# Kernel tuning notes

Hardware: AMD Instinct MI355X
Metric: run time of the kernel (lower is better)

## Reference

```python
import jax, jax.numpy as jnp
import numpy as np
import math

D_MODEL = 1024
NUM_HEADS = 16
D_K = D_MODEL // NUM_HEADS
B, S = 2, 2048


def setup_inputs() -> dict:
    key = jax.random.key(0)
    ks = jax.random.split(key, 11)
    scale = 1.0 / math.sqrt(D_MODEL)
    inp = {
        "query": jax.random.normal(ks[0], (B, S, D_MODEL), jnp.float32),
        "key": jax.random.normal(ks[1], (B, S, D_MODEL), jnp.float32),
        "value": jax.random.normal(ks[2], (B, S, D_MODEL), jnp.float32),
        "Wq": jax.random.normal(ks[3], (D_MODEL, D_MODEL), jnp.float32) * scale,
        "bq": jnp.zeros((D_MODEL,), jnp.float32),
        "Wk": jax.random.normal(ks[4], (D_MODEL, D_MODEL), jnp.float32) * scale,
        "bk": jnp.zeros((D_MODEL,), jnp.float32),
        "Wv": jax.random.normal(ks[5], (D_MODEL, D_MODEL), jnp.float32) * scale,
        "bv": jnp.zeros((D_MODEL,), jnp.float32),
        "Wo": jax.random.normal(ks[6], (D_MODEL, D_MODEL), jnp.float32) * scale,
        "bo": jnp.zeros((D_MODEL,), jnp.float32),
    }
    return inp


def reference(query, key, value, Wq, bq, Wk, bk, Wv, bv, Wo, bo):
    b, s, _ = query.shape
    # QKV projections (torch Linear: x @ W.T + b)
    Q = query @ Wq.T + bq
    K = key @ Wk.T + bk
    V = value @ Wv.T + bv
    # [b, h, s, d_k]
    Q = Q.reshape(b, s, NUM_HEADS, D_K).transpose(0, 2, 1, 3)
    K = K.reshape(b, s, NUM_HEADS, D_K).transpose(0, 2, 1, 3)
    V = V.reshape(b, s, NUM_HEADS, D_K).transpose(0, 2, 1, 3)
    score = jnp.einsum("bhqd,bhkd->bhqk", Q, K) / math.sqrt(D_K)
    attn = jax.nn.softmax(score, axis=-1)
    out = jnp.einsum("bhqk,bhkd->bhqd", attn, V)
    out = out.transpose(0, 2, 1, 3).reshape(b, s, D_MODEL)
    return out @ Wo.T + bo
```

## Files before the change

### kernel.cpp

```cpp
#include <hip/hip_runtime.h>

#define NHEADS 16
#define SEQ    2048
#define BATCH  2
#define DMODEL 1024
#define MTOT   4096

typedef __attribute__((ext_vector_type(8)))  short short8;
typedef __attribute__((ext_vector_type(4)))  float f32x4;
typedef __attribute__((ext_vector_type(16))) float f32x16;

__device__ __forceinline__ unsigned short f32_to_bf16_rn(float x) {
  unsigned int u = __float_as_uint(x);
  u += 0x7fffu + ((u >> 16) & 1u);
  return (unsigned short)(u >> 16);
}

__device__ __forceinline__ unsigned cvt_pk_bf16(float lo, float hi_) {
  unsigned r;
  asm("v_cvt_pk_bf16_f32 %0, %1, %2" : "=v"(r) : "v"(lo), "v"(hi_));
  return r;
}

__device__ __forceinline__ void permlane32_swap(unsigned &a, unsigned &b) {
  asm("v_permlane32_swap_b32 %0, %1" : "+v"(a), "+v"(b));
}

__device__ __forceinline__ void async16(void* lds, const void* g) {
  __builtin_amdgcn_global_load_lds((const __attribute__((address_space(1))) unsigned int*)g,
                                   (__attribute__((address_space(3))) unsigned int*)lds, 16, 0, 0);
}

__global__ void cvt_bf16_kernel(const float* __restrict__ x0, const float* __restrict__ x1,
                                const float* __restrict__ x2,
                                const float* __restrict__ w0, const float* __restrict__ w1,
                                const float* __restrict__ w2, const float* __restrict__ w3,
                                unsigned short* __restrict__ obase)
{
  const int e = (blockIdx.x*256 + threadIdx.x)*8;
  const float* src;
  int local;
  if (e < 3*4194304) {
    const int t = e >> 22;
    src = t==0 ? x0 : t==1 ? x1 : x2;
    local = e & (4194304-1);
    src += local;
    local += t << 22;
  } else {
    const int f = e - 3*4194304;
    const int t = f >> 20;
    src = t==0 ? w0 : t==1 ? w1 : t==2 ? w2 : w3;
    src += (f & (1048576-1));
    local = e;
  }
  const float4 v0 = *(const float4*)(src);
  const float4 v1 = *(const float4*)(src + 4);
  union { unsigned short u[8]; uint4 v; } r;
  r.u[0] = f32_to_bf16_rn(v0.x); r.u[1] = f32_to_bf16_rn(v0.y);
  r.u[2] = f32_to_bf16_rn(v0.z); r.u[3] = f32_to_bf16_rn(v0.w);
  r.u[4] = f32_to_bf16_rn(v1.x); r.u[5] = f32_to_bf16_rn(v1.y);
  r.u[6] = f32_to_bf16_rn(v1.z); r.u[7] = f32_to_bf16_rn(v1.w);
  *(uint4*)(obase + local) = r.v;
}

template<int BM>
__device__ __forceinline__ void gemm_core(const unsigned short* __restrict__ A,
                                          const unsigned short* __restrict__ W,
                                          unsigned short* sA, unsigned short* sB,
                                          int m0, int n0, f32x4 (&acc)[BM/32][4])
{
  constexpr int MI = BM/32;
  const int t = threadIdx.x;
  const int lane = t & 63;
  const int wv = t >> 6;
  const int wm = wv >> 1, wn = wv & 1;
  const int lr = lane & 15, lk = lane >> 4;

  for (int kt = 0; kt < DMODEL/64; ++kt) {
    #pragma unroll
    for (int g = 0; g < MI; ++g) {
      const int o  = g*4096 + t*16;
      const int so = o ^ (((o >> 7) & 7) << 4);
      const int row = so >> 7, colE = (so & 127) >> 1;
      async16((char*)sA + o, A + (size_t)(m0 + row)*DMODEL + kt*64 + colE);
    }
    #pragma unroll
    for (int g = 0; g < 4; ++g) {
      const int o  = g*4096 + t*16;
      const int so = o ^ (((o >> 7) & 7) << 4);
      const int row = so >> 7, colE = (so & 127) >> 1;
      async16((char*)sB + o, W + (size_t)(n0 + row)*DMODEL + kt*64 + colE);
    }
    __syncthreads();
    #pragma unroll
    for (int ks = 0; ks < 2; ++ks) {
      short8 af[MI], bf[4];
      #pragma unroll
      for (int mi = 0; mi < MI; ++mi) {
        const int row = wm*(BM/2) + mi*16 + lr;
        const int sl  = (ks*4 + lk) ^ (row & 7);
        af[mi] = *(const short8*)(sA + row*64 + sl*8);
      }
      #pragma unroll
      for (int ni = 0; ni < 4; ++ni) {
        const int row = wn*64 + ni*16 + lr;
        const int sl  = (ks*4 + lk) ^ (row & 7);
        bf[ni] = *(const short8*)(sB + row*64 + sl*8);
      }
      #pragma unroll
      for (int mi = 0; mi < MI; ++mi)
        #pragma unroll
        for (int ni = 0; ni < 4; ++ni)
          acc[mi][ni] = __builtin_amdgcn_mfma_f32_16x16x32_bf16(af[mi], bf[ni], acc[mi][ni], 0, 0, 0);
    }
    __syncthreads();
  }
}

__global__ __launch_bounds__(256, 2)
void qkv_gemm_kernel(const unsigned short* __restrict__ Xq, const unsigned short* __restrict__ Xk,
                     const unsigned short* __restrict__ Xv,
                     const unsigned short* __restrict__ Wq, const unsigned short* __restrict__ Wk,
                     const unsigned short* __restrict__ Wv,
                     const float* __restrict__ bq, const float* __restrict__ bk,
                     const float* __restrict__ bv,
                     unsigned short* __restrict__ Qp, unsigned short* __restrict__ Kp,
                     unsigned short* __restrict__ Vtp)
{
  constexpr int BM = 128;
  constexpr int MI = BM/32;
  __shared__ __align__(16) unsigned short smem[17024];
  unsigned short* sA = smem;
  unsigned short* sB = smem + 8192;

  const int m0   = blockIdx.x * BM;
  const int nabs = blockIdx.y * 128;
  const int wsel = nabs >> 10;
  const int n0   = nabs & 1023;
  const unsigned short* A = wsel==0 ? Xq : wsel==1 ? Xk : Xv;
  const unsigned short* W = wsel==0 ? Wq : wsel==1 ? Wk : Wv;
  const float* bias       = wsel==0 ? bq : wsel==1 ? bk : bv;

  f32x4 acc[MI][4];
  #pragma unroll
  for (int mi = 0; mi < MI; ++mi)
    #pragma unroll
    for (int ni = 0; ni < 4; ++ni)
      acc[mi][ni] = {0.f, 0.f, 0.f, 0.f};

  gemm_core<BM>(A, W, sA, sB, m0, n0, acc);

  const int t = threadIdx.x, lane = t & 63, wvx = t >> 6;
  const int wm = wvx >> 1, wn = wvx & 1;
  const int lr = lane & 15, lk = lane >> 4;

  if (wsel == 2) {
    #pragma unroll
    for (int ni = 0; ni < 4; ++ni) {
      const float badd = bias[n0 + wn*64 + ni*16 + lr];
      #pragma unroll
      for (int mi = 0; mi < MI; ++mi)
        #pragma unroll
        for (int r = 0; r < 4; ++r) {
          const int ml = wm*(BM/2) + mi*16 + lk*4 + r;
          smem[(wn*64 + ni*16 + lr)*132 + ml] = f32_to_bf16_rn(acc[mi][ni][r] + badd);
        }
    }
    __syncthreads();
    const int bb = m0 >> 11, s0 = m0 & 2047;
    const int jr = (t & 15)*8, nr = t >> 4;
    #pragma unroll
    for (int pass = 0; pass < 8; ++pass) {
      const int n  = pass*16 + nr;
      const int nn = n0 + n, hh = nn >> 6, d = nn & 63;
      const short8 v = *(const short8*)(smem + n*132 + jr);
      *(short8*)(Vtp + (((size_t)bb*NHEADS + hh)*64 + d)*SEQ + s0 + jr) = v;
    }
  } else {
    unsigned short* dst = wsel==0 ? Qp : Kp;
    const float qscale = (wsel == 0) ? 0.125f * 1.4426950408889634f : 1.0f;
    #pragma unroll
    for (int ni = 0; ni < 4; ++ni) {
      const int nn = n0 + wn*64 + ni*16 + lr;
      const float badd = bias[nn];
      const int hh = nn >> 6, d = nn & 63;
      #pragma unroll
      for (int mi = 0; mi < MI; ++mi) {
        #pragma unroll
        for (int r = 0; r < 4; ++r) {
          const int m = m0 + wm*(BM/2) + mi*16 + lk*4 + r;
          const int bb = m >> 11, s = m & 2047;
          const float v = (acc[mi][ni][r] + badd) * qscale;
          dst[(((size_t)bb*NHEADS + hh)*SEQ + s)*64 + d] = f32_to_bf16_rn(v);
        }
      }
    }
  }
}

__global__ __launch_bounds__(256, 2)
void attn_kernel(const unsigned short* __restrict__ Qp, const unsigned short* __restrict__ Kp,
                 const unsigned short* __restrict__ Vtp, unsigned short* __restrict__ Op)
{
  __shared__ __align__(16) unsigned short sm[3*8192];
  constexpr int NT = SEQ/64;

  const int t = threadIdx.x, lane = t & 63, w = t >> 6;
  const int lq = lane & 31, hi = lane >> 5;
  const int f   = blockIdx.x + 16*blockIdx.y + 256*blockIdx.z;
  const int wid = (f & 7)*64 + (f >> 3);
  const int qt = wid & 15, h = (wid >> 4) & 15, b = wid >> 8;

  const size_t bh = (size_t)b*NHEADS + h;
  const unsigned short* Qh = Qp  + bh*SEQ*64;
  const unsigned short* Kh = Kp  + bh*SEQ*64;
  const unsigned short* Vh = Vtp + bh*64*SEQ;
  const int q0 = qt*128 + w*32;

  short8 qf[4];
  #pragma unroll
  for (int ks = 0; ks < 4; ++ks)
    qf[ks] = *(const short8*)(Qh + (size_t)(q0 + lq)*64 + ks*16 + hi*8);

  union { unsigned u[4]; short8 s; } ones;
  #pragma unroll
  for (int i = 0; i < 4; ++i) ones.u[i] = 0x3F803F80u;

  const unsigned short* srcp;
  size_t sstride;
  if (w < 2) { srcp = Kh + (size_t)(w*32 + lq)*64 + hi*8;        sstride = 64*64; }
  else       { srcp = Vh + (size_t)((w-2)*32 + lq)*2048 + hi*8;  sstride = 64;    }

  #pragma unroll
  for (int i = 0; i < 4; ++i) async16((char*)sm + 0     + w*4096 + i*1024, srcp + i*16);
  srcp += sstride;
  #pragma unroll
  for (int i = 0; i < 4; ++i) async16((char*)sm + 16384 + w*4096 + i*1024, srcp + i*16);
  srcp += sstride;

  f32x16 o[2], ls, stA[2], stB[2];
  #pragma unroll
  for (int d = 0; d < 2; ++d)
    #pragma unroll
    for (int r = 0; r < 16; ++r) { o[d][r] = 0.f; stA[d][r] = 0.f; stB[d][r] = 0.f; }
  #pragma unroll
  for (int r = 0; r < 16; ++r) ls[r] = 0.f;

  asm volatile("s_waitcnt vmcnt(4)" ::: "memory");
  __syncthreads();
  __builtin_amdgcn_s_setprio(1);
  #pragma unroll
  for (int sub = 0; sub < 2; ++sub)
    #pragma unroll
    for (int ks = 0; ks < 4; ++ks) {
      const short8 kf = *(const short8*)(sm + (sub*4 + ks)*512 + lane*8);
      stA[sub] = __builtin_amdgcn_mfma_f32_32x32x16_bf16(kf, qf[ks], stA[sub], 0, 0, 0);
    }
  __builtin_amdgcn_s_setprio(0);

  auto body = [&](f32x16 (&cur)[2], f32x16 (&nxt)[2], int tc, int obC, int obN, int obS) {
    asm volatile("s_waitcnt vmcnt(0)" ::: "memory");
    __syncthreads();
    if (tc + 2 < NT) {
      #pragma unroll
      for (int i = 0; i < 4; ++i)
        async16((char*)sm + obS + w*4096 + i*1024, srcp + i*16);
      srcp += sstride;
    }
    if (tc + 1 < NT) {
      const unsigned short* kb = sm + (obN >> 1);
      #pragma unroll
      for (int s = 0; s < 2; ++s)
        #pragma unroll
        for (int r = 0; r < 16; ++r) nxt[s][r] = 0.f;
      __builtin_amdgcn_s_setprio(1);
      #pragma unroll
      for (int sub = 0; sub < 2; ++sub)
        #pragma unroll
        for (int ks = 0; ks < 4; ++ks) {
          const short8 kf = *(const short8*)(kb + (sub*4 + ks)*512 + lane*8);
          nxt[sub] = __builtin_amdgcn_mfma_f32_32x32x16_bf16(kf, qf[ks], nxt[sub], 0, 0, 0);
        }
      __builtin_amdgcn_s_setprio(0);
    }
    #pragma unroll
    for (int s = 0; s < 2; ++s)
      #pragma unroll
      for (int r = 0; r < 16; ++r)
        cur[s][r] = __builtin_amdgcn_exp2f(cur[s][r]);
    const unsigned short* vb = sm + (obC >> 1) + 4096;
    #pragma unroll
    for (int sub = 0; sub < 2; ++sub) {
      union { unsigned u[4]; short8 s; } pA, pB;
      {
        unsigned x0 = cvt_pk_bf16(cur[sub][0],  cur[sub][1]);
        unsigned x1 = cvt_pk_bf16(cur[sub][2],  cur[sub][3]);
        unsigned y0 = cvt_pk_bf16(cur[sub][4],  cur[sub][5]);
        unsigned y1 = cvt_pk_bf16(cur[sub][6],  cur[sub][7]);
        permlane32_swap(x0, y0);
        permlane32_swap(x1, y1);
        pA.u[0] = x0; pA.u[1] = x1; pA.u[2] = y0; pA.u[3] = y1;
        unsigned z0 = cvt_pk_bf16(cur[sub][8],  cur[sub][9]);
        unsigned z1 = cvt_pk_bf16(cur[sub][10], cur[sub][11]);
        unsigned w0 = cvt_pk_bf16(cur[sub][12], cur[sub][13]);
        unsigned w1 = cvt_pk_bf16(cur[sub][14], cur[sub][15]);
        permlane32_swap(z0, w0);
        permlane32_swap(z1, w1);
        pB.u[0] = z0; pB.u[1] = z1; pB.u[2] = w0; pB.u[3] = w1;
      }
      const short8 v00 = *(const short8*)(vb + (0*4 + 2*sub    )*512 + lane*8);
      const short8 v01 = *(const short8*)(vb + (0*4 + 2*sub + 1)*512 + lane*8);
      const short8 v10 = *(const short8*)(vb + (1*4 + 2*sub    )*512 + lane*8);
      const short8 v11 = *(const short8*)(vb + (1*4 + 2*sub + 1)*512 + lane*8);
      __builtin_amdgcn_s_setprio(1);
      o[0] = __builtin_amdgcn_mfma_f32_32x32x16_bf16(v00, pA.s, o[0], 0, 0, 0);
      o[1] = __builtin_amdgcn_mfma_f32_32x32x16_bf16(v10, pA.s, o[1], 0, 0, 0);
      ls   = __builtin_amdgcn_mfma_f32_32x32x16_bf16(ones.s, pA.s, ls, 0, 0, 0);
      o[0] = __builtin_amdgcn_mfma_f32_32x32x16_bf16(v01, pB.s, o[0], 0, 0, 0);
      o[1] = __builtin_amdgcn_mfma_f32_32x32x16_bf16(v11, pB.s, o[1], 0, 0, 0);
      ls   = __builtin_amdgcn_mfma_f32_32x32x16_bf16(ones.s, pB.s, ls, 0, 0, 0);
      __builtin_amdgcn_s_setprio(0);
    }
  };

  int obC = 0, obN = 16384, obS = 32768;
  for (int t2 = 0; t2 < NT; t2 += 2) {
    body(stA, stB, t2,     obC, obN, obS);
    int tmp = obC; obC = obN; obN = obS; obS = tmp;
    body(stB, stA, t2 + 1, obC, obN, obS);
    tmp = obC; obC = obN; obN = obS; obS = tmp;
  }

  const float inv = __builtin_amdgcn_rcpf(ls[0]);
  unsigned short* orow = Op + ((size_t)b*SEQ + q0 + lq)*DMODEL + h*64;
  #pragma unroll
  for (int dblk = 0; dblk < 2; ++dblk)
    #pragma unroll
    for (int g = 0; g < 4; ++g) {
      union { unsigned short us[4]; uint2 v; } pk;
      #pragma unroll
      for (int r = 0; r < 4; ++r) pk.us[r] = f32_to_bf16_rn(o[dblk][g*4 + r] * inv);
      *(uint2*)(orow + dblk*32 + g*8 + hi*4) = pk.v;
    }
}

__global__ __launch_bounds__(256, 2)
void oproj_gemm_kernel(const unsigned short* __restrict__ Oin, const unsigned short* __restrict__ Wo,
                       const float* __restrict__ bo, float* __restrict__ out)
{
  constexpr int BM = 64;
  constexpr int MI = BM/32;
  __shared__ __align__(16) unsigned short sA[BM*64];
  __shared__ __align__(16) unsigned short sB[128*64];
  const int m0 = blockIdx.x * BM;
  const int n0 = blockIdx.y * 128;

  f32x4 acc[MI][4];
  #pragma unroll
  for (int mi = 0; mi < MI; ++mi)
    #pragma unroll
    for (int ni = 0; ni < 4; ++ni)
      acc[mi][ni] = {0.f,0.f,0.f,0.f};

  gemm_core<BM>(Oin, Wo, sA, sB, m0, n0, acc);

  const int t = threadIdx.x, lane = t & 63, wvx = t >> 6;
  const int wm = wvx >> 1, wn = wvx & 1;
  const int lr = lane & 15, lk = lane >> 4;

  #pragma unroll
  for (int ni = 0; ni < 4; ++ni) {
    const int nn = n0 + wn*64 + ni*16 + lr;
    const float badd = bo[nn];
    #pragma unroll
    for (int mi = 0; mi < MI; ++mi)
      #pragma unroll
      for (int r = 0; r < 4; ++r) {
        const int m = m0 + wm*(BM/2) + mi*16 + lk*4 + r;
        out[(size_t)m*DMODEL + nn] = acc[mi][ni][r] + badd;
      }
  }
}

extern "C" void kernel_launch(void* const* d_in, const int* in_sizes, int n_in,
                              void* d_out, int out_size, void* d_ws, size_t ws_size,
                              hipStream_t stream) {
  const float* query = (const float*)d_in[0];
  const float* key   = (const float*)d_in[1];
  const float* value = (const float*)d_in[2];
  const float* Wq    = (const float*)d_in[3];
  const float* bq    = (const float*)d_in[4];
  const float* Wk    = (const float*)d_in[5];
  const float* bk    = (const float*)d_in[6];
  const float* Wv    = (const float*)d_in[7];
  const float* bv    = (const float*)d_in[8];
  const float* Wo    = (const float*)d_in[9];
  const float* bo    = (const float*)d_in[10];

  const size_t NX = (size_t)MTOT*DMODEL;
  const size_t NW = (size_t)DMODEL*DMODEL;
  unsigned short* w   = (unsigned short*)d_ws;
  unsigned short* Xq  = w;
  unsigned short* Xk  = Xq  + NX;
  unsigned short* Xv  = Xk  + NX;
  unsigned short* Wqp = Xv  + NX;
  unsigned short* Wkp = Wqp + NW;
  unsigned short* Wvp = Wkp + NW;
  unsigned short* Wop = Wvp + NW;
  unsigned short* Qp  = Wop + NW;
  unsigned short* Kp  = Qp  + NX;
  unsigned short* Vtp = Kp  + NX;
  unsigned short* Opb = Vtp + NX;

  cvt_bf16_kernel<<<dim3(8192), 256, 0, stream>>>(
      query, key, value, Wq, Wk, Wv, Wo, w);
  qkv_gemm_kernel<<<dim3(32, 24), 256, 0, stream>>>(
      Xq, Xk, Xv, Wqp, Wkp, Wvp, bq, bk, bv, Qp, Kp, Vtp);
  attn_kernel<<<dim3(16, 16, 2), 256, 0, stream>>>(Qp, Kp, Vtp, Opb);
  oproj_gemm_kernel<<<dim3(64, 8), 256, 0, stream>>>(Opb, Wop, bo, (float*)d_out);
}
```

Baseline: 113.0 us.

## Load K and V fragments directly from global into registers, dropping LDS staging

```diff
diff --git a/kernel.cpp b/kernel.cpp
--- a/kernel.cpp
+++ b/kernel.cpp
@@ -202,7 +202,6 @@
 void attn_kernel(const unsigned short* __restrict__ Qp, const unsigned short* __restrict__ Kp,
                  const unsigned short* __restrict__ Vtp, unsigned short* __restrict__ Op)
 {
-  __shared__ __align__(16) unsigned short sm[3*8192];
   constexpr int NT = SEQ/64;
 
   const int t = threadIdx.x, lane = t & 63, w = t >> 6;
@@ -226,109 +225,90 @@
   #pragma unroll
   for (int i = 0; i < 4; ++i) ones.u[i] = 0x3F803F80u;
 
-  const unsigned short* srcp;
-  size_t sstride;
-  if (w < 2) { srcp = Kh + (size_t)(w*32 + lq)*64 + hi*8;        sstride = 64*64; }
-  else       { srcp = Vh + (size_t)((w-2)*32 + lq)*2048 + hi*8;  sstride = 64;    }
-
-  #pragma unroll
-  for (int i = 0; i < 4; ++i) async16((char*)sm + 0     + w*4096 + i*1024, srcp + i*16);
-  srcp += sstride;
-  #pragma unroll
-  for (int i = 0; i < 4; ++i) async16((char*)sm + 16384 + w*4096 + i*1024, srcp + i*16);
-  srcp += sstride;
-
-  f32x16 o[2], ls, stA[2], stB[2];
+  f32x16 o[2], ls;
   #pragma unroll
   for (int d = 0; d < 2; ++d)
     #pragma unroll
-    for (int r = 0; r < 16; ++r) { o[d][r] = 0.f; stA[d][r] = 0.f; stB[d][r] = 0.f; }
+    for (int r = 0; r < 16; ++r) o[d][r] = 0.f;
   #pragma unroll
   for (int r = 0; r < 16; ++r) ls[r] = 0.f;
 
-  asm volatile("s_waitcnt vmcnt(4)" ::: "memory");
-  __syncthreads();
-  __builtin_amdgcn_s_setprio(1);
+  const unsigned short* krow = Kh + (size_t)lq*64 + hi*8;
+  const unsigned short* vrow = Vh + (size_t)lq*2048 + hi*8;
+
+  short8 kfA[8], kfB[8];
   #pragma unroll
   for (int sub = 0; sub < 2; ++sub)
     #pragma unroll
-    for (int ks = 0; ks < 4; ++ks) {
-      const short8 kf = *(const short8*)(sm + (sub*4 + ks)*512 + lane*8);
-      stA[sub] = __builtin_amdgcn_mfma_f32_32x32x16_bf16(kf, qf[ks], stA[sub], 0, 0, 0);
-    }
-  __builtin_amdgcn_s_setprio(0);
-
-  auto body = [&](f32x16 (&cur)[2], f32x16 (&nxt)[2], int tc, int obC, int obN, int obS) {
-    asm volatile("s_waitcnt vmcnt(0)" ::: "memory");
-    __syncthreads();
-    if (tc + 2 < NT) {
-      #pragma unroll
-      for (int i = 0; i < 4; ++i)
-        async16((char*)sm + obS + w*4096 + i*1024, srcp + i*16);
-      srcp += sstride;
-    }
-    if (tc + 1 < NT) {
-      const unsigned short* kb = sm + (obN >> 1);
-      #pragma unroll
-      for (int s = 0; s < 2; ++s)
-        #pragma unroll
-        for (int r = 0; r < 16; ++r) nxt[s][r] = 0.f;
-      __builtin_amdgcn_s_setprio(1);
-      #pragma unroll
-      for (int sub = 0; sub < 2; ++sub)
-        #pragma unroll
-        for (int ks = 0; ks < 4; ++ks) {
-          const short8 kf = *(const short8*)(kb + (sub*4 + ks)*512 + lane*8);
-          nxt[sub] = __builtin_amdgcn_mfma_f32_32x32x16_bf16(kf, qf[ks], nxt[sub], 0, 0, 0);
-        }
-      __builtin_amdgcn_s_setprio(0);
-    }
+    for (int ks = 0; ks < 4; ++ks)
+      kfA[sub*4+ks] = *(const short8*)(krow + (size_t)sub*32*64 + ks*16);
+
+  auto body = [&](short8 (&kcur)[8], short8 (&knxt)[8], int kv0) {
+    const int nkv = (kv0 + 64) & (SEQ - 1);
+    #pragma unroll
+    for (int sub = 0; sub < 2; ++sub)
+      #pragma unroll
+      for (int ks = 0; ks < 4; ++ks)
+        knxt[sub*4+ks] = *(const short8*)(krow + (size_t)(nkv + sub*32)*64 + ks*16);
+    short8 vf[8];
+    #pragma unroll
+    for (int dblk = 0; dblk < 2; ++dblk)
+      #pragma unroll
+      for (int sl = 0; sl < 4; ++sl)
+        vf[dblk*4+sl] = *(const short8*)(vrow + (size_t)dblk*32*2048 + kv0 + sl*16);
+
+    f32x16 st[2];
     #pragma unroll
     for (int s = 0; s < 2; ++s)
       #pragma unroll
+      for (int r = 0; r < 16; ++r) st[s][r] = 0.f;
+    __builtin_amdgcn_s_setprio(1);
+    #pragma unroll
+    for (int sub = 0; sub < 2; ++sub)
+      #pragma unroll
+      for (int ks = 0; ks < 4; ++ks)
+        st[sub] = __builtin_amdgcn_mfma_f32_32x32x16_bf16(kcur[sub*4+ks], qf[ks], st[sub], 0, 0, 0);
+    __builtin_amdgcn_s_setprio(0);
+
+    #pragma unroll
+    for (int s = 0; s < 2; ++s)
+      #pragma unroll
       for (int r = 0; r < 16; ++r)
-        cur[s][r] = __builtin_amdgcn_exp2f(cur[s][r]);
-    const unsigned short* vb = sm + (obC >> 1) + 4096;
+        st[s][r] = __builtin_amdgcn_exp2f(st[s][r]);
+
     #pragma unroll
     for (int sub = 0; sub < 2; ++sub) {
       union { unsigned u[4]; short8 s; } pA, pB;
       {
-        unsigned x0 = cvt_pk_bf16(cur[sub][0],  cur[sub][1]);
-        unsigned x1 = cvt_pk_bf16(cur[sub][2],  cur[sub][3]);
-        unsigned y0 = cvt_pk_bf16(cur[sub][4],  cur[sub][5]);
-        unsigned y1 = cvt_pk_bf16(cur[sub][6],  cur[sub][7]);
+        unsigned x0 = cvt_pk_bf16(st[sub][0],  st[sub][1]);
+        unsigned x1 = cvt_pk_bf16(st[sub][2],  st[sub][3]);
+        unsigned y0 = cvt_pk_bf16(st[sub][4],  st[sub][5]);
+        unsigned y1 = cvt_pk_bf16(st[sub][6],  st[sub][7]);
         permlane32_swap(x0, y0);
         permlane32_swap(x1, y1);
         pA.u[0] = x0; pA.u[1] = x1; pA.u[2] = y0; pA.u[3] = y1;
-        unsigned z0 = cvt_pk_bf16(cur[sub][8],  cur[sub][9]);
-        unsigned z1 = cvt_pk_bf16(cur[sub][10], cur[sub][11]);
-        unsigned w0 = cvt_pk_bf16(cur[sub][12], cur[sub][13]);
-        unsigned w1 = cvt_pk_bf16(cur[sub][14], cur[sub][15]);
+        unsigned z0 = cvt_pk_bf16(st[sub][8],  st[sub][9]);
+        unsigned z1 = cvt_pk_bf16(st[sub][10], st[sub][11]);
+        unsigned w0 = cvt_pk_bf16(st[sub][12], st[sub][13]);
+        unsigned w1 = cvt_pk_bf16(st[sub][14], st[sub][15]);
         permlane32_swap(z0, w0);
         permlane32_swap(z1, w1);
         pB.u[0] = z0; pB.u[1] = z1; pB.u[2] = w0; pB.u[3] = w1;
       }
-      const short8 v00 = *(const short8*)(vb + (0*4 + 2*sub    )*512 + lane*8);
-      const short8 v01 = *(const short8*)(vb + (0*4 + 2*sub + 1)*512 + lane*8);
-      const short8 v10 = *(const short8*)(vb + (1*4 + 2*sub    )*512 + lane*8);
-      const short8 v11 = *(const short8*)(vb + (1*4 + 2*sub + 1)*512 + lane*8);
       __builtin_amdgcn_s_setprio(1);
-      o[0] = __builtin_amdgcn_mfma_f32_32x32x16_bf16(v00, pA.s, o[0], 0, 0, 0);
-      o[1] = __builtin_amdgcn_mfma_f32_32x32x16_bf16(v10, pA.s, o[1], 0, 0, 0);
-      ls   = __builtin_amdgcn_mfma_f32_32x32x16_bf16(ones.s, pA.s, ls, 0, 0, 0);
-      o[0] = __builtin_amdgcn_mfma_f32_32x32x16_bf16(v01, pB.s, o[0], 0, 0, 0);
-      o[1] = __builtin_amdgcn_mfma_f32_32x32x16_bf16(v11, pB.s, o[1], 0, 0, 0);
-      ls   = __builtin_amdgcn_mfma_f32_32x32x16_bf16(ones.s, pB.s, ls, 0, 0, 0);
+      o[0] = __builtin_amdgcn_mfma_f32_32x32x16_bf16(vf[0*4 + sub*2    ], pA.s, o[0], 0, 0, 0);
+      o[1] = __builtin_amdgcn_mfma_f32_32x32x16_bf16(vf[1*4 + sub*2    ], pA.s, o[1], 0, 0, 0);
+      ls   = __builtin_amdgcn_mfma_f32_32x32x16_bf16(ones.s,             pA.s, ls,   0, 0, 0);
+      o[0] = __builtin_amdgcn_mfma_f32_32x32x16_bf16(vf[0*4 + sub*2 + 1], pB.s, o[0], 0, 0, 0);
+      o[1] = __builtin_amdgcn_mfma_f32_32x32x16_bf16(vf[1*4 + sub*2 + 1], pB.s, o[1], 0, 0, 0);
+      ls   = __builtin_amdgcn_mfma_f32_32x32x16_bf16(ones.s,             pB.s, ls,   0, 0, 0);
       __builtin_amdgcn_s_setprio(0);
     }
   };
 
-  int obC = 0, obN = 16384, obS = 32768;
   for (int t2 = 0; t2 < NT; t2 += 2) {
-    body(stA, stB, t2,     obC, obN, obS);
-    int tmp = obC; obC = obN; obN = obS; obS = tmp;
-    body(stB, stA, t2 + 1, obC, obN, obS);
-    tmp = obC; obC = obN; obN = obS; obS = tmp;
+    body(kfA, kfB, t2*64);
+    body(kfB, kfA, t2*64 + 64);
   }
 
   const float inv = __builtin_amdgcn_rcpf(ls[0]);
```

New measurement: 186.4 us. 65.0% more time.
